# Optimization experiments

Measured on AMD Instinct MI355X. Metric: run time of the kernel, lower is better.

## Reference

```python
import jax, jax.numpy as jnp
import numpy as np

B, IN, OUT = 64, 4096, 1024
BETA, THRESH, RESET = 0.98, 0.4, 0.0
A_POS, A_NEG, TRACE_DECAY = 0.005, 0.004, 0.85


def setup_inputs() -> dict:
    key = jax.random.key(0)
    k1, k2 = jax.random.split(key)
    in_spikes = jax.random.uniform(k1, (B, IN), dtype=jnp.float32)  # spike input currents
    weight = jax.random.normal(k2, (OUT, IN), dtype=jnp.float32) * 0.02  # nn.Linear weight [out,in]
    membrane = jnp.zeros((B, OUT), dtype=jnp.float32)
    trace_pre = jnp.zeros((IN,), dtype=jnp.float32)
    trace_post = jnp.zeros((OUT,), dtype=jnp.float32)
    return {"in_spikes": in_spikes, "weight": weight, "membrane": membrane,
            "trace_pre": trace_pre, "trace_post": trace_post}


def reference(in_spikes, weight, membrane, trace_pre, trace_post):
    # weighted input: [B,OUT]
    weighted = in_spikes @ weight.T
    # LIF neuron update
    mem = membrane * BETA + weighted
    spikes = (mem > THRESH).astype(mem.dtype)
    mem = jnp.where(spikes > 0, RESET, mem)
    # STDP trace updates (trace_pre broadcasts [IN] -> [B,IN], as in the torch code)
    tp = jnp.clip(trace_pre * TRACE_DECAY + in_spikes, 0.0, 1.0)   # [B,IN]
    tq = jnp.clip(trace_post * TRACE_DECAY + spikes, 0.0, 1.0)     # [B,OUT]
    # potentiation - depression = (a_pos - a_neg) * outer(tp, tq); summed over batch
    # and transposed -> [OUT,IN]. Expressed as one einsum instead of materializing
    # the [B,IN,OUT] tensor (algebraically identical).
    dw = (A_POS - A_NEG) * jnp.einsum('bi,bo->oi', tp, tq)
    w_new = jnp.clip(weight + dw, -0.1, 0.5)
    # module returns out_spikes; state updates returned too for verification
    return spikes, mem, w_new, tp, tq
```

## Files before the change

kernel.cpp:

```cpp
#include <hip/hip_runtime.h>


#define B_    64
#define IN_   4096
#define OUT_  1024
#define SPLITS 32
#define KC    128
#define BK    64

static constexpr int OFF_SPIKES = 0;
static constexpr int OFF_MEM    = B_ * OUT_;
static constexpr int OFF_W      = 2 * B_ * OUT_;
static constexpr int OFF_TP     = OFF_W + OUT_ * IN_;
static constexpr int OFF_TQ     = OFF_TP + B_ * IN_;

typedef short          s16x8 __attribute__((ext_vector_type(8)));
typedef unsigned short u16x8 __attribute__((ext_vector_type(8)));
typedef float          f32x4 __attribute__((ext_vector_type(4)));

__device__ __forceinline__ unsigned short bf16_rne(float x) {
  unsigned u = __float_as_uint(x);
  return (unsigned short)((u + 0x7fffu + ((u >> 16) & 1u)) >> 16);
}

__global__ __launch_bounds__(256) void k_gemm1(const float* __restrict__ A,
                                               const float* __restrict__ Wt,
                                               float* __restrict__ part) {
  const int nb   = blockIdx.x;
  const int ks   = blockIdx.y;
  const int t    = threadIdx.x;
  const int lane = t & 63;
  const int w    = t >> 6;

  __shared__ unsigned short Ah[64][64], Al[64][64], Wh[64][64], Wl[64][64];

  f32x4 acc[4];
#pragma unroll
  for (int bt = 0; bt < 4; ++bt) acc[bt] = (f32x4){0.f, 0.f, 0.f, 0.f};

#pragma unroll
  for (int c = 0; c < 2; ++c) {
    const int k0 = ks * KC + c * BK;

#pragma unroll
    for (int s = t; s < 512; s += 256) {
      const int r  = s >> 3;
      const int j  = s & 7;
      const int jc = (j ^ (r & 7)) << 3;

      const float* ap = A + (size_t)r * IN_ + k0 + j * 8;
      const float4 a0 = *reinterpret_cast<const float4*>(ap);
      const float4 a1 = *reinterpret_cast<const float4*>(ap + 4);
      const float  af[8] = {a0.x, a0.y, a0.z, a0.w, a1.x, a1.y, a1.z, a1.w};
      u16x8 ahi, alo;
#pragma unroll
      for (int e = 0; e < 8; ++e) {
        const unsigned short h = bf16_rne(af[e]);
        ahi[e] = h;
        alo[e] = bf16_rne(af[e] - __uint_as_float(((unsigned)h) << 16));
      }
      *reinterpret_cast<u16x8*>(&Ah[r][jc]) = ahi;
      *reinterpret_cast<u16x8*>(&Al[r][jc]) = alo;

      const float* wp = Wt + (size_t)(nb * 64 + r) * IN_ + k0 + j * 8;
      const float4 w0 = *reinterpret_cast<const float4*>(wp);
      const float4 w1 = *reinterpret_cast<const float4*>(wp + 4);
      const float  wf[8] = {w0.x, w0.y, w0.z, w0.w, w1.x, w1.y, w1.z, w1.w};
      u16x8 whi, wlo;
#pragma unroll
      for (int e = 0; e < 8; ++e) {
        const unsigned short h = bf16_rne(wf[e]);
        whi[e] = h;
        wlo[e] = bf16_rne(wf[e] - __uint_as_float(((unsigned)h) << 16));
      }
      *reinterpret_cast<u16x8*>(&Wh[r][jc]) = whi;
      *reinterpret_cast<u16x8*>(&Wl[r][jc]) = wlo;
    }
    __syncthreads();

#pragma unroll
    for (int kk = 0; kk < 2; ++kk) {
      const int c4 = kk * 4 + (lane >> 4);
      const int jc = (c4 ^ (lane & 7)) << 3;
      const int nloc = w * 16 + (lane & 15);

      const s16x8 whi = *reinterpret_cast<const s16x8*>(&Wh[nloc][jc]);
      const s16x8 wlo = *reinterpret_cast<const s16x8*>(&Wl[nloc][jc]);
#pragma unroll
      for (int bt = 0; bt < 4; ++bt) {
        const int bloc = bt * 16 + (lane & 15);
        const s16x8 ahi = *reinterpret_cast<const s16x8*>(&Ah[bloc][jc]);
        const s16x8 alo = *reinterpret_cast<const s16x8*>(&Al[bloc][jc]);
        acc[bt] = __builtin_amdgcn_mfma_f32_16x16x32_bf16(ahi, whi, acc[bt], 0, 0, 0);
        acc[bt] = __builtin_amdgcn_mfma_f32_16x16x32_bf16(ahi, wlo, acc[bt], 0, 0, 0);
        acc[bt] = __builtin_amdgcn_mfma_f32_16x16x32_bf16(alo, whi, acc[bt], 0, 0, 0);
      }
    }
    if (c == 0) __syncthreads();
  }

  const int n_g = nb * 64 + w * 16 + (lane & 15);
#pragma unroll
  for (int bt = 0; bt < 4; ++bt) {
#pragma unroll
    for (int reg = 0; reg < 4; ++reg) {
      const int b = bt * 16 + (lane >> 4) * 4 + reg;
      part[((size_t)(ks * 64 + b)) * OUT_ + n_g] = acc[bt][reg];
    }
  }
}

__global__ __launch_bounds__(256) void k_post(const float* __restrict__ part,
                                              const float* __restrict__ membrane,
                                              const float* __restrict__ trace_post,
                                              const float* __restrict__ in_spikes,
                                              const float* __restrict__ trace_pre,
                                              float* __restrict__ out) {
  const int t = blockIdx.x * 256 + threadIdx.x;
  const int b = t >> 10;
  const int n = t & (OUT_ - 1);

  float s0 = 0.f, s1 = 0.f, s2 = 0.f, s3 = 0.f;
#pragma unroll
  for (int ks = 0; ks < SPLITS; ks += 4) {
    s0 += part[((size_t)((ks + 0) * B_ + b)) * OUT_ + n];
    s1 += part[((size_t)((ks + 1) * B_ + b)) * OUT_ + n];
    s2 += part[((size_t)((ks + 2) * B_ + b)) * OUT_ + n];
    s3 += part[((size_t)((ks + 3) * B_ + b)) * OUT_ + n];
  }
  const float weighted = (s0 + s1) + (s2 + s3);

  const float mem   = fmaf(membrane[t], 0.98f, weighted);
  const float spike = (mem > 0.4f) ? 1.0f : 0.0f;
  const float memo  = (spike > 0.0f) ? 0.0f : mem;
  float tq = fmaf(trace_post[n], 0.85f, spike);
  tq = fminf(fmaxf(tq, 0.0f), 1.0f);

  out[OFF_SPIKES + t] = spike;
  out[OFF_MEM    + t] = memo;
  out[OFF_TQ     + t] = tq;

  const int i4 = t & (IN_ / 4 - 1);
  const float4 x  = reinterpret_cast<const float4*>(in_spikes)[t];
  const float4 tr = reinterpret_cast<const float4*>(trace_pre)[i4];
  float4 r;
  r.x = fminf(fmaxf(fmaf(tr.x, 0.85f, x.x), 0.0f), 1.0f);
  r.y = fminf(fmaxf(fmaf(tr.y, 0.85f, x.y), 0.0f), 1.0f);
  r.z = fminf(fmaxf(fmaf(tr.z, 0.85f, x.z), 0.0f), 1.0f);
  r.w = fminf(fmaxf(fmaf(tr.w, 0.85f, x.w), 0.0f), 1.0f);
  reinterpret_cast<float4*>(out + OFF_TP)[t] = r;
}

__global__ __launch_bounds__(256) void k_wnew(const float* __restrict__ weight,
                                              const float* __restrict__ tp,
                                              const float* __restrict__ tq,
                                              float* __restrict__ wout) {
  const int i0 = blockIdx.x * 64;
  const int o0 = blockIdx.y * 64;

  __shared__ float tpl[64][68];
  __shared__ float tql[64][68];
  {
    const int c4 = threadIdx.x & 15;
    const int rr = threadIdx.x >> 4;
#pragma unroll
    for (int r = 0; r < 4; ++r) {
      const int b = rr + r * 16;
      *reinterpret_cast<float4*>(&tpl[b][c4 * 4]) =
          *reinterpret_cast<const float4*>(tp + (size_t)b * IN_  + i0 + c4 * 4);
      *reinterpret_cast<float4*>(&tql[b][c4 * 4]) =
          *reinterpret_cast<const float4*>(tq + (size_t)b * OUT_ + o0 + c4 * 4);
    }
  }
  __syncthreads();

  const int il = threadIdx.x & 15;
  const int ol = threadIdx.x >> 4;

  float acc[4][4];
#pragma unroll
  for (int u = 0; u < 4; ++u)
#pragma unroll
    for (int v = 0; v < 4; ++v) acc[u][v] = 0.f;

#pragma unroll 4
  for (int b = 0; b < 64; ++b) {
    const float4 tpv = *reinterpret_cast<const float4*>(&tpl[b][il * 4]);
    const float4 tqv = *reinterpret_cast<const float4*>(&tql[b][ol * 4]);
    const float tp4[4] = {tpv.x, tpv.y, tpv.z, tpv.w};
    const float tq4[4] = {tqv.x, tqv.y, tqv.z, tqv.w};
#pragma unroll
    for (int u = 0; u < 4; ++u)
#pragma unroll
      for (int v = 0; v < 4; ++v)
        acc[u][v] = fmaf(tq4[u], tp4[v], acc[u][v]);
  }

  const float cdw = (float)(0.005 - 0.004);
#pragma unroll
  for (int u = 0; u < 4; ++u) {
    const int o = o0 + ol * 4 + u;
    const float4 wv = *reinterpret_cast<const float4*>(
        weight + (size_t)o * IN_ + i0 + il * 4);
    float4 r;
    r.x = fminf(fmaxf(fmaf(cdw, acc[u][0], wv.x), -0.1f), 0.5f);
    r.y = fminf(fmaxf(fmaf(cdw, acc[u][1], wv.y), -0.1f), 0.5f);
    r.z = fminf(fmaxf(fmaf(cdw, acc[u][2], wv.z), -0.1f), 0.5f);
    r.w = fminf(fmaxf(fmaf(cdw, acc[u][3], wv.w), -0.1f), 0.5f);
    *reinterpret_cast<float4*>(wout + (size_t)o * IN_ + i0 + il * 4) = r;
  }
}

extern "C" void kernel_launch(void* const* d_in, const int* in_sizes, int n_in,
                              void* d_out, int out_size, void* d_ws, size_t ws_size,
                              hipStream_t stream) {
  const float* in_spikes  = (const float*)d_in[0];
  const float* weight     = (const float*)d_in[1];
  const float* membrane   = (const float*)d_in[2];
  const float* trace_pre  = (const float*)d_in[3];
  const float* trace_post = (const float*)d_in[4];
  float* out = (float*)d_out;

  float* part = out + OFF_W;

  k_gemm1<<<dim3(16, SPLITS), 256, 0, stream>>>(in_spikes, weight, part);
  k_post <<<dim3(256),        256, 0, stream>>>(part, membrane, trace_post,
                                                in_spikes, trace_pre, out);
  k_wnew <<<dim3(64, 16),     256, 0, stream>>>(weight, out + OFF_TP,
                                                out + OFF_TQ, out + OFF_W);
}
```

Measured before the change: 93.64 us.

## Fuse GEMM, LIF update and weight update into one cooperative kernel

```diff
diff --git a/kernel.cpp b/kernel.cpp
--- a/kernel.cpp
+++ b/kernel.cpp
@@ -1,4 +1,7 @@
 #include <hip/hip_runtime.h>
+#include <hip/hip_cooperative_groups.h>
+
+namespace cg = cooperative_groups;
 
 
 #define B_    64
@@ -23,191 +26,213 @@
   return (unsigned short)((u + 0x7fffu + ((u >> 16) & 1u)) >> 16);
 }
 
-__global__ __launch_bounds__(256) void k_gemm1(const float* __restrict__ A,
+struct SharedU {
+  union {
+    struct { unsigned short Ah[64][64], Al[64][64], Wh[64][64], Wl[64][64]; } g;
+    struct { float tpl[64][68], tql[64][68]; } w;
+  };
+};
+
+__global__ __launch_bounds__(256) void k_fused(const float* __restrict__ A,
                                                const float* __restrict__ Wt,
+                                               const float* __restrict__ membrane,
+                                               const float* __restrict__ trace_pre,
+                                               const float* __restrict__ trace_post,
+                                               float* __restrict__ out,
                                                float* __restrict__ part) {
-  const int nb   = blockIdx.x;
-  const int ks   = blockIdx.y;
+  cg::grid_group grid = cg::this_grid();
+  __shared__ SharedU sh;
+
+  const int bid  = blockIdx.x;
   const int t    = threadIdx.x;
   const int lane = t & 63;
   const int w    = t >> 6;
 
-  __shared__ unsigned short Ah[64][64], Al[64][64], Wh[64][64], Wl[64][64];
-
-  f32x4 acc[4];
-#pragma unroll
-  for (int bt = 0; bt < 4; ++bt) acc[bt] = (f32x4){0.f, 0.f, 0.f, 0.f};
-
-#pragma unroll
-  for (int c = 0; c < 2; ++c) {
-    const int k0 = ks * KC + c * BK;
-
-#pragma unroll
-    for (int s = t; s < 512; s += 256) {
-      const int r  = s >> 3;
-      const int j  = s & 7;
-      const int jc = (j ^ (r & 7)) << 3;
-
-      const float* ap = A + (size_t)r * IN_ + k0 + j * 8;
-      const float4 a0 = *reinterpret_cast<const float4*>(ap);
-      const float4 a1 = *reinterpret_cast<const float4*>(ap + 4);
-      const float  af[8] = {a0.x, a0.y, a0.z, a0.w, a1.x, a1.y, a1.z, a1.w};
-      u16x8 ahi, alo;
-#pragma unroll
-      for (int e = 0; e < 8; ++e) {
-        const unsigned short h = bf16_rne(af[e]);
-        ahi[e] = h;
-        alo[e] = bf16_rne(af[e] - __uint_as_float(((unsigned)h) << 16));
-      }
-      *reinterpret_cast<u16x8*>(&Ah[r][jc]) = ahi;
-      *reinterpret_cast<u16x8*>(&Al[r][jc]) = alo;
-
-      const float* wp = Wt + (size_t)(nb * 64 + r) * IN_ + k0 + j * 8;
-      const float4 w0 = *reinterpret_cast<const float4*>(wp);
-      const float4 w1 = *reinterpret_cast<const float4*>(wp + 4);
-      const float  wf[8] = {w0.x, w0.y, w0.z, w0.w, w1.x, w1.y, w1.z, w1.w};
-      u16x8 whi, wlo;
-#pragma unroll
-      for (int e = 0; e < 8; ++e) {
-        const unsigned short h = bf16_rne(wf[e]);
-        whi[e] = h;
-        wlo[e] = bf16_rne(wf[e] - __uint_as_float(((unsigned)h) << 16));
-      }
-      *reinterpret_cast<u16x8*>(&Wh[r][jc]) = whi;
-      *reinterpret_cast<u16x8*>(&Wl[r][jc]) = wlo;
-    }
-    __syncthreads();
-
-#pragma unroll
-    for (int kk = 0; kk < 2; ++kk) {
-      const int c4 = kk * 4 + (lane >> 4);
-      const int jc = (c4 ^ (lane & 7)) << 3;
-      const int nloc = w * 16 + (lane & 15);
-
-      const s16x8 whi = *reinterpret_cast<const s16x8*>(&Wh[nloc][jc]);
-      const s16x8 wlo = *reinterpret_cast<const s16x8*>(&Wl[nloc][jc]);
-#pragma unroll
-      for (int bt = 0; bt < 4; ++bt) {
-        const int bloc = bt * 16 + (lane & 15);
-        const s16x8 ahi = *reinterpret_cast<const s16x8*>(&Ah[bloc][jc]);
-        const s16x8 alo = *reinterpret_cast<const s16x8*>(&Al[bloc][jc]);
-        acc[bt] = __builtin_amdgcn_mfma_f32_16x16x32_bf16(ahi, whi, acc[bt], 0, 0, 0);
-        acc[bt] = __builtin_amdgcn_mfma_f32_16x16x32_bf16(ahi, wlo, acc[bt], 0, 0, 0);
-        acc[bt] = __builtin_amdgcn_mfma_f32_16x16x32_bf16(alo, whi, acc[bt], 0, 0, 0);
-      }
-    }
-    if (c == 0) __syncthreads();
+  {
+    const int nb = bid & 15;
+    const int ks = bid >> 4;
+
+    f32x4 acc[4];
+#pragma unroll
+    for (int bt = 0; bt < 4; ++bt) acc[bt] = (f32x4){0.f, 0.f, 0.f, 0.f};
+
+#pragma unroll
+    for (int c = 0; c < 2; ++c) {
+      const int k0 = ks * KC + c * BK;
+      if (c) __syncthreads();
+
+#pragma unroll
+      for (int s = t; s < 512; s += 256) {
+        const int r  = s >> 3;
+        const int j  = s & 7;
+        const int jc = (j ^ (r & 7)) << 3;
+
+        const float* ap = A + (size_t)r * IN_ + k0 + j * 8;
+        const float4 a0 = *reinterpret_cast<const float4*>(ap);
+        const float4 a1 = *reinterpret_cast<const float4*>(ap + 4);
+        const float  af[8] = {a0.x, a0.y, a0.z, a0.w, a1.x, a1.y, a1.z, a1.w};
+        u16x8 ahi, alo;
+#pragma unroll
+        for (int e = 0; e < 8; ++e) {
+          const unsigned short h = bf16_rne(af[e]);
+          ahi[e] = h;
+          alo[e] = bf16_rne(af[e] - __uint_as_float(((unsigned)h) << 16));
+        }
+        *reinterpret_cast<u16x8*>(&sh.g.Ah[r][jc]) = ahi;
+        *reinterpret_cast<u16x8*>(&sh.g.Al[r][jc]) = alo;
+
+        const float* wp = Wt + (size_t)(nb * 64 + r) * IN_ + k0 + j * 8;
+        const float4 w0 = *reinterpret_cast<const float4*>(wp);
+        const float4 w1 = *reinterpret_cast<const float4*>(wp + 4);
+        const float  wf[8] = {w0.x, w0.y, w0.z, w0.w, w1.x, w1.y, w1.z, w1.w};
+        u16x8 whi, wlo;
+#pragma unroll
+        for (int e = 0; e < 8; ++e) {
+          const unsigned short h = bf16_rne(wf[e]);
+          whi[e] = h;
+          wlo[e] = bf16_rne(wf[e] - __uint_as_float(((unsigned)h) << 16));
+        }
+        *reinterpret_cast<u16x8*>(&sh.g.Wh[r][jc]) = whi;
+        *reinterpret_cast<u16x8*>(&sh.g.Wl[r][jc]) = wlo;
+      }
+      __syncthreads();
+
+#pragma unroll
+      for (int kk = 0; kk < 2; ++kk) {
+        const int c4 = kk * 4 + (lane >> 4);
+        const int jc = (c4 ^ (lane & 7)) << 3;
+        const int nloc = w * 16 + (lane & 15);
+
+        const s16x8 whi = *reinterpret_cast<const s16x8*>(&sh.g.Wh[nloc][jc]);
+        const s16x8 wlo = *reinterpret_cast<const s16x8*>(&sh.g.Wl[nloc][jc]);
+#pragma unroll
+        for (int bt = 0; bt < 4; ++bt) {
+          const int bloc = bt * 16 + (lane & 15);
+          const s16x8 ahi = *reinterpret_cast<const s16x8*>(&sh.g.Ah[bloc][jc]);
+          const s16x8 alo = *reinterpret_cast<const s16x8*>(&sh.g.Al[bloc][jc]);
+          acc[bt] = __builtin_amdgcn_mfma_f32_16x16x32_bf16(ahi, whi, acc[bt], 0, 0, 0);
+          acc[bt] = __builtin_amdgcn_mfma_f32_16x16x32_bf16(ahi, wlo, acc[bt], 0, 0, 0);
+          acc[bt] = __builtin_amdgcn_mfma_f32_16x16x32_bf16(alo, whi, acc[bt], 0, 0, 0);
+        }
+      }
+    }
+
+    const int n_g = nb * 64 + w * 16 + (lane & 15);
+#pragma unroll
+    for (int bt = 0; bt < 4; ++bt) {
+#pragma unroll
+      for (int reg = 0; reg < 4; ++reg) {
+        const int b = bt * 16 + (lane >> 4) * 4 + reg;
+        part[((size_t)(ks * 64 + b)) * OUT_ + n_g] = acc[bt][reg];
+      }
+    }
   }
 
-  const int n_g = nb * 64 + w * 16 + (lane & 15);
-#pragma unroll
-  for (int bt = 0; bt < 4; ++bt) {
-#pragma unroll
-    for (int reg = 0; reg < 4; ++reg) {
-      const int b = bt * 16 + (lane >> 4) * 4 + reg;
-      part[((size_t)(ks * 64 + b)) * OUT_ + n_g] = acc[bt][reg];
+  grid.sync();
+
+  {
+    const int g = bid * 256 + t;
+    if (g < B_ * OUT_) {
+      const int b = g >> 10;
+      const int n = g & (OUT_ - 1);
+
+      float s0 = 0.f, s1 = 0.f, s2 = 0.f, s3 = 0.f;
+#pragma unroll
+      for (int ks = 0; ks < SPLITS; ks += 4) {
+        s0 += part[((size_t)((ks + 0) * B_ + b)) * OUT_ + n];
+        s1 += part[((size_t)((ks + 1) * B_ + b)) * OUT_ + n];
+        s2 += part[((size_t)((ks + 2) * B_ + b)) * OUT_ + n];
+        s3 += part[((size_t)((ks + 3) * B_ + b)) * OUT_ + n];
+      }
+      const float weighted = (s0 + s1) + (s2 + s3);
+
+      const float mem   = fmaf(membrane[g], 0.98f, weighted);
+      const float spike = (mem > 0.4f) ? 1.0f : 0.0f;
+      const float memo  = (spike > 0.0f) ? 0.0f : mem;
+      float tq = fmaf(trace_post[n], 0.85f, spike);
+      tq = fminf(fmaxf(tq, 0.0f), 1.0f);
+
+      out[OFF_SPIKES + g] = spike;
+      out[OFF_MEM    + g] = memo;
+      out[OFF_TQ     + g] = tq;
+
+      const int i4 = g & (IN_ / 4 - 1);
+      const float4 x  = reinterpret_cast<const float4*>(A)[g];
+      const float4 tr = reinterpret_cast<const float4*>(trace_pre)[i4];
+      float4 r;
+      r.x = fminf(fmaxf(fmaf(tr.x, 0.85f, x.x), 0.0f), 1.0f);
+      r.y = fminf(fmaxf(fmaf(tr.y, 0.85f, x.y), 0.0f), 1.0f);
+      r.z = fminf(fmaxf(fmaf(tr.z, 0.85f, x.z), 0.0f), 1.0f);
+      r.w = fminf(fmaxf(fmaf(tr.w, 0.85f, x.w), 0.0f), 1.0f);
+      reinterpret_cast<float4*>(out + OFF_TP)[g] = r;
     }
   }
-}
-
-__global__ __launch_bounds__(256) void k_post(const float* __restrict__ part,
-                                              const float* __restrict__ membrane,
-                                              const float* __restrict__ trace_post,
-                                              const float* __restrict__ in_spikes,
-                                              const float* __restrict__ trace_pre,
-                                              float* __restrict__ out) {
-  const int t = blockIdx.x * 256 + threadIdx.x;
-  const int b = t >> 10;
-  const int n = t & (OUT_ - 1);
-
-  float s0 = 0.f, s1 = 0.f, s2 = 0.f, s3 = 0.f;
-#pragma unroll
-  for (int ks = 0; ks < SPLITS; ks += 4) {
-    s0 += part[((size_t)((ks + 0) * B_ + b)) * OUT_ + n];
-    s1 += part[((size_t)((ks + 1) * B_ + b)) * OUT_ + n];
-    s2 += part[((size_t)((ks + 2) * B_ + b)) * OUT_ + n];
-    s3 += part[((size_t)((ks + 3) * B_ + b)) * OUT_ + n];
-  }
-  const float weighted = (s0 + s1) + (s2 + s3);
-
-  const float mem   = fmaf(membrane[t], 0.98f, weighted);
-  const float spike = (mem > 0.4f) ? 1.0f : 0.0f;
-  const float memo  = (spike > 0.0f) ? 0.0f : mem;
-  float tq = fmaf(trace_post[n], 0.85f, spike);
-  tq = fminf(fmaxf(tq, 0.0f), 1.0f);
-
-  out[OFF_SPIKES + t] = spike;
-  out[OFF_MEM    + t] = memo;
-  out[OFF_TQ     + t] = tq;
-
-  const int i4 = t & (IN_ / 4 - 1);
-  const float4 x  = reinterpret_cast<const float4*>(in_spikes)[t];
-  const float4 tr = reinterpret_cast<const float4*>(trace_pre)[i4];
-  float4 r;
-  r.x = fminf(fmaxf(fmaf(tr.x, 0.85f, x.x), 0.0f), 1.0f);
-  r.y = fminf(fmaxf(fmaf(tr.y, 0.85f, x.y), 0.0f), 1.0f);
-  r.z = fminf(fmaxf(fmaf(tr.z, 0.85f, x.z), 0.0f), 1.0f);
-  r.w = fminf(fmaxf(fmaf(tr.w, 0.85f, x.w), 0.0f), 1.0f);
-  reinterpret_cast<float4*>(out + OFF_TP)[t] = r;
-}
-
-__global__ __launch_bounds__(256) void k_wnew(const float* __restrict__ weight,
-                                              const float* __restrict__ tp,
-                                              const float* __restrict__ tq,
-                                              float* __restrict__ wout) {
-  const int i0 = blockIdx.x * 64;
-  const int o0 = blockIdx.y * 64;
-
-  __shared__ float tpl[64][68];
-  __shared__ float tql[64][68];
+
+  grid.sync();
+
   {
-    const int c4 = threadIdx.x & 15;
-    const int rr = threadIdx.x >> 4;
+    const float* tp = out + OFF_TP;
+    const float* tq = out + OFF_TQ;
+    float* wout = out + OFF_W;
+
+    const int i0 = (bid & 63) * 64;
+    const int c4 = t & 15;
+    const int rr = t >> 4;
 #pragma unroll
     for (int r = 0; r < 4; ++r) {
       const int b = rr + r * 16;
-      *reinterpret_cast<float4*>(&tpl[b][c4 * 4]) =
-          *reinterpret_cast<const float4*>(tp + (size_t)b * IN_  + i0 + c4 * 4);
-      *reinterpret_cast<float4*>(&tql[b][c4 * 4]) =
-          *reinterpret_cast<const float4*>(tq + (size_t)b * OUT_ + o0 + c4 * 4);
-    }
-  }
-  __syncthreads();
-
-  const int il = threadIdx.x & 15;
-  const int ol = threadIdx.x >> 4;
-
-  float acc[4][4];
-#pragma unroll
-  for (int u = 0; u < 4; ++u)
-#pragma unroll
-    for (int v = 0; v < 4; ++v) acc[u][v] = 0.f;
+      *reinterpret_cast<float4*>(&sh.w.tpl[b][c4 * 4]) =
+          *reinterpret_cast<const float4*>(tp + (size_t)b * IN_ + i0 + c4 * 4);
+    }
+
+    const int il = t & 15;
+    const int ol = t >> 4;
+
+#pragma unroll
+    for (int half = 0; half < 2; ++half) {
+      const int o0 = ((bid >> 6) + half * 8) * 64;
+      if (half) __syncthreads();
+#pragma unroll
+      for (int r = 0; r < 4; ++r) {
+        const int b = rr + r * 16;
+        *reinterpret_cast<float4*>(&sh.w.tql[b][c4 * 4]) =
+            *reinterpret_cast<const float4*>(tq + (size_t)b * OUT_ + o0 + c4 * 4);
+      }
+      __syncthreads();
+
+      float acc[4][4];
+#pragma unroll
+      for (int u = 0; u < 4; ++u)
+#pragma unroll
+        for (int v = 0; v < 4; ++v) acc[u][v] = 0.f;
 
 #pragma unroll 4
-  for (int b = 0; b < 64; ++b) {
-    const float4 tpv = *reinterpret_cast<const float4*>(&tpl[b][il * 4]);
-    const float4 tqv = *reinterpret_cast<const float4*>(&tql[b][ol * 4]);
-    const float tp4[4] = {tpv.x, tpv.y, tpv.z, tpv.w};
-    const float tq4[4] = {tqv.x, tqv.y, tqv.z, tqv.w};
-#pragma unroll
-    for (int u = 0; u < 4; ++u)
-#pragma unroll
-      for (int v = 0; v < 4; ++v)
-        acc[u][v] = fmaf(tq4[u], tp4[v], acc[u][v]);
-  }
-
-  const float cdw = (float)(0.005 - 0.004);
-#pragma unroll
-  for (int u = 0; u < 4; ++u) {
-    const int o = o0 + ol * 4 + u;
-    const float4 wv = *reinterpret_cast<const float4*>(
-        weight + (size_t)o * IN_ + i0 + il * 4);
-    float4 r;
-    r.x = fminf(fmaxf(fmaf(cdw, acc[u][0], wv.x), -0.1f), 0.5f);
-    r.y = fminf(fmaxf(fmaf(cdw, acc[u][1], wv.y), -0.1f), 0.5f);
-    r.z = fminf(fmaxf(fmaf(cdw, acc[u][2], wv.z), -0.1f), 0.5f);
-    r.w = fminf(fmaxf(fmaf(cdw, acc[u][3], wv.w), -0.1f), 0.5f);
-    *reinterpret_cast<float4*>(wout + (size_t)o * IN_ + i0 + il * 4) = r;
+      for (int b = 0; b < 64; ++b) {
+        const float4 tpv = *reinterpret_cast<const float4*>(&sh.w.tpl[b][il * 4]);
+        const float4 tqv = *reinterpret_cast<const float4*>(&sh.w.tql[b][ol * 4]);
+        const float tp4[4] = {tpv.x, tpv.y, tpv.z, tpv.w};
+        const float tq4[4] = {tqv.x, tqv.y, tqv.z, tqv.w};
+#pragma unroll
+        for (int u = 0; u < 4; ++u)
+#pragma unroll
+          for (int v = 0; v < 4; ++v)
+            acc[u][v] = fmaf(tq4[u], tp4[v], acc[u][v]);
+      }
+
+      const float cdw = (float)(0.005 - 0.004);
+#pragma unroll
+      for (int u = 0; u < 4; ++u) {
+        const int o = o0 + ol * 4 + u;
+        const float4 wv = *reinterpret_cast<const float4*>(
+            Wt + (size_t)o * IN_ + i0 + il * 4);
+        float4 r;
+        r.x = fminf(fmaxf(fmaf(cdw, acc[u][0], wv.x), -0.1f), 0.5f);
+        r.y = fminf(fmaxf(fmaf(cdw, acc[u][1], wv.y), -0.1f), 0.5f);
+        r.z = fminf(fmaxf(fmaf(cdw, acc[u][2], wv.z), -0.1f), 0.5f);
+        r.w = fminf(fmaxf(fmaf(cdw, acc[u][3], wv.w), -0.1f), 0.5f);
+        *reinterpret_cast<float4*>(wout + (size_t)o * IN_ + i0 + il * 4) = r;
+      }
+    }
   }
 }
 
@@ -223,9 +248,9 @@
 
   float* part = out + OFF_W;
 
-  k_gemm1<<<dim3(16, SPLITS), 256, 0, stream>>>(in_spikes, weight, part);
-  k_post <<<dim3(256),        256, 0, stream>>>(part, membrane, trace_post,
-                                                in_spikes, trace_pre, out);
-  k_wnew <<<dim3(64, 16),     256, 0, stream>>>(weight, out + OFF_TP,
-                                                out + OFF_TQ, out + OFF_W);
+  void* args[] = {(void*)&in_spikes, (void*)&weight, (void*)&membrane,
+                  (void*)&trace_pre, (void*)&trace_post, (void*)&out,
+                  (void*)&part};
+  hipLaunchCooperativeKernel((const void*)k_fused, dim3(512), dim3(256),
+                             args, 0, stream);
 }
```

After: 216.7 us. 2.31x slower.
